# Optimization experiments

Measured on AMD Instinct MI355X. Metric: run time of the kernel, lower is better.

The kernel has to match this reference:

```python
import jax, jax.numpy as jnp
import numpy as np

NUM_HEADS = 16
HEAD_DIM = 64
HIDDEN = NUM_HEADS * HEAD_DIM  # 1024


def get_rel_pos(q_size, k_size, rel_pos):
    # q_size == k_size here and rel_pos already has 2*size-1 rows, so the
    # F.interpolate(mode='linear') resize in the original is an identity.
    # relative_coords = q - k + (k_size - 1)  (scale factors are 1.0)
    coords = jnp.arange(q_size)[:, None] - jnp.arange(k_size)[None, :] + (k_size - 1)
    return rel_pos[coords]  # [q_size, k_size, head_dim]


def setup_inputs() -> dict:
    key = jax.random.key(0)
    ks = jax.random.split(key, 7)
    B, H, W = 4, 56, 28
    inp = {
        "hidden_states": jax.random.normal(ks[0], (B, H, W, HIDDEN), jnp.float32),
        "qkv_w": jax.random.normal(ks[1], (3 * HIDDEN, HIDDEN), jnp.float32) * 0.02,
        "qkv_b": jax.random.normal(ks[2], (3 * HIDDEN,), jnp.float32) * 0.02,
        "proj_w": jax.random.normal(ks[3], (HIDDEN, HIDDEN), jnp.float32) * 0.02,
        "proj_b": jax.random.normal(ks[4], (HIDDEN,), jnp.float32) * 0.02,
        "rel_pos_h": jax.random.normal(ks[5], (2 * H - 1, HEAD_DIM), jnp.float32) * 0.02,
        "rel_pos_w": jax.random.normal(ks[6], (2 * W - 1, HEAD_DIM), jnp.float32) * 0.02,
    }
    return inp


def reference(hidden_states, qkv_w, qkv_b, proj_w, proj_b, rel_pos_h, rel_pos_w):
    B, H, W, C = hidden_states.shape
    N = H * W
    scale = HEAD_DIM ** -0.5

    # qkv projection -> [3, B*heads, N, head_dim]
    qkv = hidden_states @ qkv_w.T + qkv_b
    qkv = qkv.reshape(B, N, 3, NUM_HEADS, HEAD_DIM).transpose(2, 0, 3, 1, 4)
    qkv = qkv.reshape(3, B * NUM_HEADS, N, HEAD_DIM)
    query, key_, value = qkv[0], qkv[1], qkv[2]

    # scaled dot-product scores, fully materialized as in the original
    attn = jnp.einsum('bqd,bkd->bqk', query * scale, key_)  # [B*heads, N, N]

    # decomposed relative position bias
    Rh = get_rel_pos(H, H, rel_pos_h)  # [H, H, d]
    Rw = get_rel_pos(W, W, rel_pos_w)  # [W, W, d]
    q_r = query.reshape(B * NUM_HEADS, H, W, HEAD_DIM)
    rel_h = jnp.einsum('bhwc,hkc->bhwk', q_r, Rh)  # [B*heads, H, W, H]
    rel_w = jnp.einsum('bhwc,wkc->bhwk', q_r, Rw)  # [B*heads, H, W, W]
    attn = attn.reshape(B * NUM_HEADS, H, W, H, W)
    attn = attn + rel_h[:, :, :, :, None] + rel_w[:, :, :, None, :]
    attn = attn.reshape(B * NUM_HEADS, N, N)

    attn = jax.nn.softmax(attn.astype(jnp.float32), axis=-1).astype(query.dtype)

    out = jnp.einsum('bqk,bkd->bqd', attn, value)
    out = out.reshape(B, NUM_HEADS, H, W, HEAD_DIM).transpose(0, 2, 3, 1, 4)
    out = out.reshape(B, H, W, C)
    out = out @ proj_w.T + proj_b
    return out
```

## Files before the change

kernel.cpp:

```cpp
#include <hip/hip_runtime.h>
#include <hip/hip_bf16.h>
#include <stdint.h>

typedef __bf16 bf16;
typedef __bf16 bf16x2 __attribute__((ext_vector_type(2)));
typedef __bf16 bf16x4 __attribute__((ext_vector_type(4)));
typedef __bf16 bf16x8 __attribute__((ext_vector_type(8)));
typedef float f32x4 __attribute__((ext_vector_type(4)));

#define AS1 __attribute__((address_space(1)))
#define AS3 __attribute__((address_space(3)))

static __device__ __forceinline__ void async_cp16(const bf16* g, bf16* l) {
    __builtin_amdgcn_global_load_lds((const AS1 void*)g, (AS3 void*)l, 16, 0, 0);
}

static __device__ __forceinline__ bf16x4 cvt4(f32x4 v) {
    bf16x4 r;
    r[0] = (bf16)v[0]; r[1] = (bf16)v[1]; r[2] = (bf16)v[2]; r[3] = (bf16)v[3];
    return r;
}

static __device__ __forceinline__ float fast_exp2(float x) {
#if __has_builtin(__builtin_amdgcn_exp2f)
    return __builtin_amdgcn_exp2f(x);
#else
    return __expf(x * 0.69314718056f);
#endif
}

__global__ __launch_bounds__(256) void cvt_kernel(
    const float* __restrict__ src, bf16* __restrict__ dst, int n4) {
    int i = blockIdx.x * 256 + threadIdx.x;
    const int stride = gridDim.x * 256;
    for (; i < n4; i += stride)
        ((bf16x4*)dst)[i] = cvt4(((const f32x4*)src)[i]);
}

__global__ __launch_bounds__(256) void build_kone(bf16* __restrict__ Kone) {
    const int idx = blockIdx.x * 256 + threadIdx.x;
    if (idx >= 6400) return;
    const int key = idx >> 2, chunk = idx & 3;
    const int hk = key / 28;
    const int wk = key - hk * 28;
    const int kt = key >> 6;
    const int ha = (kt << 6) / 28;
    const int jw = 27 - wk;
    const int jh = 31 - (hk - ha);
    bf16x8 v;
#pragma unroll
    for (int e = 0; e < 8; e++) {
        const int j = chunk * 8 + e;
        v[e] = (j == jw || j == jh) ? (bf16)1.0f : (bf16)0.0f;
    }
    *(bf16x8*)&Kone[key * 32 + chunk * 8] = v;
}

__global__ __launch_bounds__(256) void zero_pads(
    bf16* __restrict__ Kb, bf16* __restrict__ Vt) {
    const int idx = blockIdx.x * 256 + threadIdx.x;
    if (idx >= 32768) return;
    const int g = idx >> 9, r = idx & 511;
    bf16x8 z = {};
    if (r < 256) {
        *(bf16x8*)&Kb[((size_t)g * 1600 + 1568) * 64 + r * 8] = z;
    } else {
        const int rr = r - 256;
        *(bf16x8*)&Vt[((size_t)g * 64 + (rr >> 2)) * 1600 + 1568 + (rr & 3) * 8] = z;
    }
}


#define QKV_EPILOGUE()                                                        \
    for (int nt = 0; nt < 4; nt++) {                                          \
        const int n_ = n0 + wn + nt * 16 + lm;                                \
        const float bv = bias[n_];                                            \
        const int s = n_ >> 10, rem = n_ & 1023;                              \
        const int h = rem >> 6, d = rem & 63;                                 \
        const float qsc = (s == 0) ? 0.18033688011112042f : 1.0f;             \
        for (int mt = 0; mt < 4; mt++) {                                      \
            for (int r = 0; r < 4; r++) {                                     \
                const int m_ = m0 + wm + mt * 16 + quad * 4 + r;              \
                const int b = m_ / 1568;                                      \
                const int pix = m_ - b * 1568;                                \
                const int g = b * 16 + h;                                     \
                const bf16 v = (bf16)((acc[mt][nt][r] + bv) * qsc);           \
                if (s == 0)      Qb[((size_t)g * 1568 + pix) * 64 + d] = v;   \
                else if (s == 1) Kb[((size_t)g * 1600 + pix) * 64 + d] = v;   \
                else {                                                        \
                    const int lk = pix & 31;                                  \
                    const int ppix = (pix & ~31) | ((lk & 15) << 1) | (lk >> 4); \
                    Vt[((size_t)g * 64 + d) * 1600 + ppix] = v;               \
                }                                                             \
            }                                                                 \
        }                                                                     \
    }

__global__ __launch_bounds__(256) void qkv_gemm_bf16(
    const bf16* __restrict__ A, const bf16* __restrict__ W,
    const float* __restrict__ bias, bf16* __restrict__ Qb,
    bf16* __restrict__ Kb, bf16* __restrict__ Vt) {
    __shared__ bf16 As[128 * 32];
    __shared__ bf16 Bs[128 * 32];
    const int t = threadIdx.x;
    const int wid = t >> 6, lane = t & 63;
    const int m0 = blockIdx.x * 128, n0 = blockIdx.y * 128;
    const int wm = (wid & 1) * 64, wn = (wid >> 1) * 64;
    const int r_i = lane >> 2, c8 = (lane & 3) * 8;
    const int lm = lane & 15, quad = lane >> 4;

    f32x4 acc[4][4] = {};
    for (int k0 = 0; k0 < 1024; k0 += 32) {
        __syncthreads();
        for (int i = 0; i < 2; i++) {
            const int blk = wid * 2 + i;
            async_cp16(A + (size_t)(m0 + blk * 16 + r_i) * 1024 + k0 + c8, As + blk * 512);
            async_cp16(W + (size_t)(n0 + blk * 16 + r_i) * 1024 + k0 + c8, Bs + blk * 512);
        }
        __syncthreads();
        bf16x8 af[4], bfr[4];
        for (int x = 0; x < 4; x++) {
            af[x]  = *(const bf16x8*)&As[(wm + x * 16 + lm) * 32 + quad * 8];
            bfr[x] = *(const bf16x8*)&Bs[(wn + x * 16 + lm) * 32 + quad * 8];
        }
        for (int mt = 0; mt < 4; mt++)
            for (int nt = 0; nt < 4; nt++)
                acc[mt][nt] = __builtin_amdgcn_mfma_f32_16x16x32_bf16(af[mt], bfr[nt], acc[mt][nt], 0, 0, 0);
    }
    QKV_EPILOGUE()
}

__global__ __launch_bounds__(256) void qkv_gemm_f32(
    const float* __restrict__ A, const float* __restrict__ W,
    const float* __restrict__ bias, bf16* __restrict__ Qb,
    bf16* __restrict__ Kb, bf16* __restrict__ Vt) {
    __shared__ bf16 As[128 * 32];
    __shared__ bf16 Bs[128 * 32];
    const int t = threadIdx.x;
    const int wid = t >> 6, lane = t & 63;
    const int m0 = blockIdx.x * 128, n0 = blockIdx.y * 128;
    const int wm = (wid & 1) * 64, wn = (wid >> 1) * 64;
    const int lm = lane & 15, quad = lane >> 4;

    f32x4 acc[4][4] = {};
    for (int k0 = 0; k0 < 1024; k0 += 32) {
        __syncthreads();
        for (int i = 0; i < 4; i++) {
            const int idx = t + i * 256;
            const int row = idx >> 3, c4 = (idx & 7) * 4;
            const f32x4 av = *(const f32x4*)&A[(size_t)(m0 + row) * 1024 + k0 + c4];
            const f32x4 wv = *(const f32x4*)&W[(size_t)(n0 + row) * 1024 + k0 + c4];
            *(bf16x4*)&As[row * 32 + c4] = cvt4(av);
            *(bf16x4*)&Bs[row * 32 + c4] = cvt4(wv);
        }
        __syncthreads();
        bf16x8 af[4], bfr[4];
        for (int x = 0; x < 4; x++) {
            af[x]  = *(const bf16x8*)&As[(wm + x * 16 + lm) * 32 + quad * 8];
            bfr[x] = *(const bf16x8*)&Bs[(wn + x * 16 + lm) * 32 + quad * 8];
        }
        for (int mt = 0; mt < 4; mt++)
            for (int nt = 0; nt < 4; nt++)
                acc[mt][nt] = __builtin_amdgcn_mfma_f32_16x16x32_bf16(af[mt], bfr[nt], acc[mt][nt], 0, 0, 0);
    }
    QKV_EPILOGUE()
}

__global__ __launch_bounds__(256) void flash_attn(
    const bf16* __restrict__ Qb, const bf16* __restrict__ Kb,
    const bf16* __restrict__ Vt, const float* __restrict__ rph,
    const float* __restrict__ rpw, const bf16* __restrict__ Kone,
    bf16* __restrict__ AO) {
    const int x = blockIdx.x;
    const int xcd = x & 7, j = x >> 3;
    const int g = xcd * 8 + j / 25;
    const int qblk = j - (j / 25) * 25;
    const int q0 = qblk * 64;
    const int hqb = q0 / 28;

    __shared__ __align__(16) char smem[51200];
    bf16* Th = (bf16*)smem;
    const char* ThC = (const char*)smem;
    char* B = smem + 8192;
    bf16* Qs  = (bf16*)(B + 32768);
    bf16* RPh = (bf16*)(B + 0);
    bf16* RPw = (bf16*)(B + 9216);
    float* TwF = (float*)(B + 18432);
    bf16* TwS = (bf16*)(B + 33280);

    const int t = threadIdx.x, wid = t >> 6, lane = t & 63;
    const int lm = lane & 15, quad = lane >> 4;
    const int qbase_l = wid * 16 + quad * 4;
    const int swz = (lm & 7) << 4;
    const int l3 = lane >> 3, l7 = lane & 7;
    const int swe = ((l7 ^ l3) << 3);

    const bf16* kSrc[2];
    const bf16* vSrc[2];
#pragma unroll
    for (int i = 0; i < 2; i++) {
        kSrc[i] = Kb + ((size_t)g * 1600 + wid * 16 + i * 8 + l3) * 64 + swe;
        vSrc[i] = Vt + ((size_t)g * 64 + wid * 16 + i * 8 + l3) * 1600 + swe;
    }

    for (int c = t; c < 512; c += 256) {
        const int row = c >> 3, col = (c & 7) * 8;
        const int qg = min(q0 + row, 1567);
        *(bf16x8*)&Qs[row * 72 + col] =
            *(const bf16x8*)&Qb[((size_t)g * 1568 + qg) * 64 + col];
    }
    for (int c = t; c < 1024; c += 256) {
        const int row = c >> 4, col = (c & 15) * 4;
        const int rg = min(hqb + row, 110);
        *(bf16x4*)&RPh[row * 72 + col] = cvt4(*(const f32x4*)&rph[rg * 64 + col]);
    }
    __syncthreads();

    const int qrow_l = wid * 16 + lm;
    const bf16x8 qf0 = *(const bf16x8*)&Qs[qrow_l * 72 + quad * 8];
    const bf16x8 qf1 = *(const bf16x8*)&Qs[qrow_l * 72 + 32 + quad * 8];
    const int qgl = min(q0 + qrow_l, 1567);
    const int thb2 = (qrow_l * 64 + (qgl / 28 - hqb) + 54) * 2;

    for (int c = t; c < 1024; c += 256) {
        const int row = c >> 4, col = (c & 15) * 4;
        const int rg = min(row, 54);
        *(bf16x4*)&RPw[row * 72 + col] = cvt4(*(const f32x4*)&rpw[rg * 64 + col]);
    }
    f32x4 acch[4];
#pragma unroll
    for (int nt = 0; nt < 4; nt++) {
        const bf16x8 b0 = *(const bf16x8*)&RPh[(nt * 16 + lm) * 72 + quad * 8];
        const bf16x8 b1 = *(const bf16x8*)&RPh[(nt * 16 + lm) * 72 + 32 + quad * 8];
        f32x4 a = {};
        a = __builtin_amdgcn_mfma_f32_16x16x32_bf16(qf0, b0, a, 0, 0, 0);
        a = __builtin_amdgcn_mfma_f32_16x16x32_bf16(qf1, b1, a, 0, 0, 0);
        acch[nt] = a;
    }
    __syncthreads();

#pragma unroll
    for (int nt = 0; nt < 4; nt++) {
        const int c = nt * 16 + lm;
        if (c < 59) {
#pragma unroll
            for (int r = 0; r < 4; r++)
                Th[(qbase_l + r) * 64 + c + 2] = (bf16)(acch[nt][r] * 8.0f);
        }
    }
    if (lm == 0) {
#pragma unroll
        for (int r = 0; r < 4; r++) {
            Th[(qbase_l + r) * 64 + 0] = (bf16)0.0f;
            Th[(qbase_l + r) * 64 + 1] = (bf16)0.0f;
        }
    }
#pragma unroll
    for (int nt = 0; nt < 4; nt++) {
        const bf16x8 b0 = *(const bf16x8*)&RPw[(nt * 16 + lm) * 72 + quad * 8];
        const bf16x8 b1 = *(const bf16x8*)&RPw[(nt * 16 + lm) * 72 + 32 + quad * 8];
        f32x4 a = {};
        a = __builtin_amdgcn_mfma_f32_16x16x32_bf16(qf0, b0, a, 0, 0, 0);
        a = __builtin_amdgcn_mfma_f32_16x16x32_bf16(qf1, b1, a, 0, 0, 0);
        const int c = nt * 16 + lm;
        if (c < 55) {
#pragma unroll
            for (int r = 0; r < 4; r++)
                TwF[(qbase_l + r) * 58 + c] = a[r] * 8.0f;
        }
    }
    __syncthreads();

    {
        const int row = t >> 2, chunk = t & 3;
        const int qg = min(q0 + row, 1567);
        const int wq = qg % 28;
        const float* src = &TwF[row * 58 + wq];
        bf16x8 v;
        if (chunk < 3) {
#pragma unroll
            for (int e = 0; e < 8; e++) v[e] = (bf16)src[chunk * 8 + e];
        } else {
#pragma unroll
            for (int e = 0; e < 4; e++) v[e] = (bf16)src[24 + e];
#pragma unroll
            for (int e = 4; e < 8; e++) v[e] = (bf16)0.0f;
        }
        *(bf16x8*)&TwS[row * 32 + chunk * 8] = v;
    }
    __syncthreads();

    const bf16x8 qt_mine = *(const bf16x8*)&TwS[qrow_l * 32 + quad * 8];

#pragma unroll
    for (int i = 0; i < 2; i++) {
        async_cp16(kSrc[i], (bf16*)(B + (wid * 2 + i) * 1024));
        async_cp16(vSrc[i], (bf16*)(B + 16384 + (wid * 2 + i) * 1024));
        kSrc[i] += 4096;
        vSrc[i] += 64;
    }
    const bf16* kop = Kone + lm * 32 + quad * 8;
    bf16x8 ko[4];
#pragma unroll
    for (int f = 0; f < 4; f++) ko[f] = *(const bf16x8*)(kop + f * 512);
    __syncthreads();

    f32x4 o[4] = {};
    f32x4 lsum = {};
    const f32x4 zero4 = {};
    bf16x8 ones;
#pragma unroll
    for (int i = 0; i < 8; i++) ones[i] = (bf16)1.0f;

    bf16* P0w = (bf16*)(B + 32768) + wid * 640;
    bf16* P1w = (bf16*)(B + 37888) + wid * 640;

    int curo = 0;
    for (int kt = 0; kt < 25; kt++) {
        bf16x8 qf2 = qt_mine;
        if (quad == 3) {
            const int ha = (kt << 6) / 28;
            const char* tp = ThC + (thb2 - (ha << 1));
            qf2[4] = *(const bf16*)(tp);
            qf2[5] = *(const bf16*)(tp + 2);
            qf2[6] = *(const bf16*)(tp + 4);
            qf2[7] = *(const bf16*)(tp + 6);
        }

        if (kt < 24) {
            const int nxto = curo ^ 8192;
#pragma unroll
            for (int i = 0; i < 2; i++) {
                async_cp16(kSrc[i], (bf16*)(B + nxto + (wid * 2 + i) * 1024));
                async_cp16(vSrc[i], (bf16*)(B + 16384 + nxto + (wid * 2 + i) * 1024));
                kSrc[i] += 4096;
                vSrc[i] += 64;
            }
        }

        __builtin_amdgcn_s_setprio(1);
        f32x4 s[4];
#pragma unroll
        for (int f = 0; f < 4; f++)
            s[f] = __builtin_amdgcn_mfma_f32_16x16x32_bf16(qf2, ko[f], zero4, 0, 0, 0);
        {
            const char* KsB = B + curo;
            const int x0 = (quad * 16) ^ swz;
#pragma unroll
            for (int f = 0; f < 4; f++) {
                const char* rp = KsB + (f * 16 + lm) * 128;
                const bf16x8 ka = *(const bf16x8*)(rp + x0);
                const bf16x8 kb2 = *(const bf16x8*)(rp + (x0 ^ 64));
                s[f] = __builtin_amdgcn_mfma_f32_16x16x32_bf16(qf0, ka, s[f], 0, 0, 0);
                s[f] = __builtin_amdgcn_mfma_f32_16x16x32_bf16(qf1, kb2, s[f], 0, 0, 0);
            }
        }
        __builtin_amdgcn_s_setprio(0);

        if (kt < 24) {
            kop += 2048;
#pragma unroll
            for (int f = 0; f < 4; f++) ko[f] = *(const bf16x8*)(kop + f * 512);
        }

        if (kt == 24) {
#pragma unroll
            for (int r = 0; r < 4; r++) { s[2][r] = -30000.0f; s[3][r] = -30000.0f; }
        }

#pragma unroll
        for (int r = 0; r < 4; r++) {
            const float a0 = fast_exp2(s[0][r]);
            const float a1 = fast_exp2(s[1][r]);
            bf16x2 pp; pp[0] = (bf16)a0; pp[1] = (bf16)a1;
            *(bf16x2*)&P0w[(quad * 4 + r) * 40 + lm * 2] = pp;
            const float b0 = fast_exp2(s[2][r]);
            const float b1 = fast_exp2(s[3][r]);
            bf16x2 qq; qq[0] = (bf16)b0; qq[1] = (bf16)b1;
            *(bf16x2*)&P1w[(quad * 4 + r) * 40 + lm * 2] = qq;
        }
        __asm__ volatile("s_waitcnt lgkmcnt(0)" ::: "memory");
        const bf16x8 pf0 = *(const bf16x8*)&P0w[lm * 40 + quad * 8];
        const bf16x8 pf1 = *(const bf16x8*)&P1w[lm * 40 + quad * 8];
        lsum = __builtin_amdgcn_mfma_f32_16x16x32_bf16(pf0, ones, lsum, 0, 0, 0);
        lsum = __builtin_amdgcn_mfma_f32_16x16x32_bf16(pf1, ones, lsum, 0, 0, 0);
        __builtin_amdgcn_s_setprio(1);
        {
            const char* VsB = B + 16384 + curo;
#pragma unroll
            for (int dt = 0; dt < 4; dt++) {
                const bf16x8 vf = *(const bf16x8*)(VsB + (dt * 16 + lm) * 128 +
                                                   ((quad * 16) ^ swz));
                o[dt] = __builtin_amdgcn_mfma_f32_16x16x32_bf16(pf0, vf, o[dt], 0, 0, 0);
            }
#pragma unroll
            for (int dt = 0; dt < 4; dt++) {
                const bf16x8 vf = *(const bf16x8*)(VsB + (dt * 16 + lm) * 128 +
                                                   ((64 + quad * 16) ^ swz));
                o[dt] = __builtin_amdgcn_mfma_f32_16x16x32_bf16(pf1, vf, o[dt], 0, 0, 0);
            }
        }
        __builtin_amdgcn_s_setprio(0);

        if (kt < 24) {
            __syncthreads();
            curo ^= 8192;
        }
    }

    if (q0 + wid * 16 < 1568) {
        const int bo = g >> 4, hh = g & 15;
#pragma unroll
        for (int r = 0; r < 4; r++) {
            const float inv = 1.0f / lsum[r];
            const size_t base = ((size_t)bo * 1568 + q0 + qbase_l + r) * 1024 + hh * 64;
#pragma unroll
            for (int dt = 0; dt < 4; dt++)
                AO[base + dt * 16 + lm] = (bf16)(o[dt][r] * inv);
        }
    }
}

__global__ __launch_bounds__(256) void proj_gemm_bf16(
    const bf16* __restrict__ A, const bf16* __restrict__ W,
    const float* __restrict__ bias, float* __restrict__ out) {
    __shared__ bf16 As[128 * 32];
    __shared__ bf16 Bs[128 * 32];
    const int t = threadIdx.x;
    const int wid = t >> 6, lane = t & 63;
    const int m0 = blockIdx.x * 128, n0 = blockIdx.y * 128;
    const int wm = (wid & 1) * 64, wn = (wid >> 1) * 64;
    const int r_i = lane >> 2, c8 = (lane & 3) * 8;
    const int lm = lane & 15, quad = lane >> 4;

    f32x4 acc[4][4] = {};
    for (int k0 = 0; k0 < 1024; k0 += 32) {
        __syncthreads();
        for (int i = 0; i < 2; i++) {
            const int blk = wid * 2 + i;
            async_cp16(A + (size_t)(m0 + blk * 16 + r_i) * 1024 + k0 + c8, As + blk * 512);
            async_cp16(W + (size_t)(n0 + blk * 16 + r_i) * 1024 + k0 + c8, Bs + blk * 512);
        }
        __syncthreads();
        bf16x8 af[4], bfr[4];
        for (int x = 0; x < 4; x++) {
            af[x]  = *(const bf16x8*)&As[(wm + x * 16 + lm) * 32 + quad * 8];
            bfr[x] = *(const bf16x8*)&Bs[(wn + x * 16 + lm) * 32 + quad * 8];
        }
        for (int mt = 0; mt < 4; mt++)
            for (int nt = 0; nt < 4; nt++)
                acc[mt][nt] = __builtin_amdgcn_mfma_f32_16x16x32_bf16(af[mt], bfr[nt], acc[mt][nt], 0, 0, 0);
    }
    for (int nt = 0; nt < 4; nt++) {
        const int n_ = n0 + wn + nt * 16 + lm;
        const float bv = bias[n_];
        for (int mt = 0; mt < 4; mt++)
            for (int r = 0; r < 4; r++) {
                const int m_ = m0 + wm + mt * 16 + quad * 4 + r;
                out[(size_t)m_ * 1024 + n_] = acc[mt][nt][r] + bv;
            }
    }
}

__global__ __launch_bounds__(256) void proj_gemm_f32(
    const bf16* __restrict__ A, const float* __restrict__ W,
    const float* __restrict__ bias, float* __restrict__ out) {
    __shared__ bf16 As[128 * 32];
    __shared__ bf16 Bs[128 * 32];
    const int t = threadIdx.x;
    const int wid = t >> 6, lane = t & 63;
    const int m0 = blockIdx.x * 128, n0 = blockIdx.y * 128;
    const int wm = (wid & 1) * 64, wn = (wid >> 1) * 64;
    const int r_i = lane >> 2, c8 = (lane & 3) * 8;
    const int lm = lane & 15, quad = lane >> 4;

    f32x4 acc[4][4] = {};
    for (int k0 = 0; k0 < 1024; k0 += 32) {
        __syncthreads();
        for (int i = 0; i < 2; i++) {
            const int blk = wid * 2 + i;
            async_cp16(A + (size_t)(m0 + blk * 16 + r_i) * 1024 + k0 + c8, As + blk * 512);
        }
        for (int i = 0; i < 4; i++) {
            const int idx = t + i * 256;
            const int row = idx >> 3, c4 = (idx & 7) * 4;
            const f32x4 wv = *(const f32x4*)&W[(size_t)(n0 + row) * 1024 + k0 + c4];
            *(bf16x4*)&Bs[row * 32 + c4] = cvt4(wv);
        }
        __syncthreads();
        bf16x8 af[4], bfr[4];
        for (int x = 0; x < 4; x++) {
            af[x]  = *(const bf16x8*)&As[(wm + x * 16 + lm) * 32 + quad * 8];
            bfr[x] = *(const bf16x8*)&Bs[(wn + x * 16 + lm) * 32 + quad * 8];
        }
        for (int mt = 0; mt < 4; mt++)
            for (int nt = 0; nt < 4; nt++)
                acc[mt][nt] = __builtin_amdgcn_mfma_f32_16x16x32_bf16(af[mt], bfr[nt], acc[mt][nt], 0, 0, 0);
    }
    for (int nt = 0; nt < 4; nt++) {
        const int n_ = n0 + wn + nt * 16 + lm;
        const float bv = bias[n_];
        for (int mt = 0; mt < 4; mt++)
            for (int r = 0; r < 4; r++) {
                const int m_ = m0 + wm + mt * 16 + quad * 4 + r;
                out[(size_t)m_ * 1024 + n_] = acc[mt][nt][r] + bv;
            }
    }
}

extern "C" void kernel_launch(void* const* d_in, const int* in_sizes, int n_in,
                              void* d_out, int out_size, void* d_ws, size_t ws_size,
                              hipStream_t stream) {
    const float* hs     = (const float*)d_in[0];
    const float* qkv_w  = (const float*)d_in[1];
    const float* qkv_b  = (const float*)d_in[2];
    const float* proj_w = (const float*)d_in[3];
    const float* proj_b = (const float*)d_in[4];
    const float* rph    = (const float*)d_in[5];
    const float* rpw    = (const float*)d_in[6];
    float* out = (float*)d_out;

    const size_t GQ  = (size_t)64 * 1568 * 64;
    const size_t GKP = (size_t)64 * 1600 * 64;
    const size_t N_KONE = (size_t)1600 * 32;
    const size_t N_HS = (size_t)6272 * 1024;
    const size_t N_QW = (size_t)3072 * 1024;
    const size_t N_PW = (size_t)1024 * 1024;
    bf16* Qb = (bf16*)d_ws;
    bf16* Kb = Qb + GQ;
    bf16* Vt = Kb + GKP;
    bf16* AO = Vt + GKP;
    bf16* Kone = AO + GQ;
    bf16* hs_bf    = Kone + N_KONE;
    bf16* qkvw_bf  = hs_bf + N_HS;
    bf16* projw_bf = qkvw_bf + N_QW;
    const size_t need = (2 * GQ + 2 * GKP + N_KONE + N_HS + N_QW + N_PW) * sizeof(bf16);

    if (ws_size >= need) {
        build_kone<<<25, 256, 0, stream>>>(Kone);
        zero_pads<<<128, 256, 0, stream>>>(Kb, Vt);
        cvt_kernel<<<512, 256, 0, stream>>>(hs, hs_bf, (int)(N_HS / 4));
        cvt_kernel<<<512, 256, 0, stream>>>(qkv_w, qkvw_bf, (int)(N_QW / 4));
        cvt_kernel<<<256, 256, 0, stream>>>(proj_w, projw_bf, (int)(N_PW / 4));
        qkv_gemm_bf16<<<dim3(49, 24), 256, 0, stream>>>(hs_bf, qkvw_bf, qkv_b, Qb, Kb, Vt);
        flash_attn<<<1600, 256, 0, stream>>>(Qb, Kb, Vt, rph, rpw, Kone, AO);
        proj_gemm_bf16<<<dim3(49, 8), 256, 0, stream>>>(AO, projw_bf, proj_b, out);
    } else {
        build_kone<<<25, 256, 0, stream>>>(Kone);
        zero_pads<<<128, 256, 0, stream>>>(Kb, Vt);
        qkv_gemm_f32<<<dim3(49, 24), 256, 0, stream>>>(hs, qkv_w, qkv_b, Qb, Kb, Vt);
        flash_attn<<<1600, 256, 0, stream>>>(Qb, Kb, Vt, rph, rpw, Kone, AO);
        proj_gemm_f32<<<dim3(49, 8), 256, 0, stream>>>(AO, proj_w, proj_b, out);
    }
}
```

Baseline: 355.1 us.

## Swizzle GEMM block order across XCDs and drop per-head K/V padding

The QKV and projection GEMMs switch to a 1D grid whose block index is remapped so that consecutive tiles land on the same XCD, aiming to improve L2 reuse of A/W tiles. The K and V^T buffers lose their 1600-row per-head padding and use a 1568 stride, with only a small slack region zeroed at the very end. Attention tail tiles now read the next head's rows instead of zeros, which is correct only if those keys are masked; in exchange the per-group zeroing work is reduced to a single tiny launch.

```diff
diff --git a/kernel.cpp b/kernel.cpp
--- a/kernel.cpp
+++ b/kernel.cpp
@@ -56,18 +56,12 @@
     *(bf16x8*)&Kone[key * 32 + chunk * 8] = v;
 }
 
-__global__ __launch_bounds__(256) void zero_pads(
-    bf16* __restrict__ Kb, bf16* __restrict__ Vt) {
-    const int idx = blockIdx.x * 256 + threadIdx.x;
-    if (idx >= 32768) return;
-    const int g = idx >> 9, r = idx & 511;
+__global__ __launch_bounds__(256) void zero_slack(
+    bf16* __restrict__ a, bf16* __restrict__ b) {
+    const int i = threadIdx.x;
     bf16x8 z = {};
-    if (r < 256) {
-        *(bf16x8*)&Kb[((size_t)g * 1600 + 1568) * 64 + r * 8] = z;
-    } else {
-        const int rr = r - 256;
-        *(bf16x8*)&Vt[((size_t)g * 64 + (rr >> 2)) * 1600 + 1568 + (rr & 3) * 8] = z;
-    }
+    *(bf16x8*)&a[i * 8] = z;
+    *(bf16x8*)&b[i * 8] = z;
 }
 
 
@@ -86,15 +80,16 @@
                 const int g = b * 16 + h;                                     \
                 const bf16 v = (bf16)((acc[mt][nt][r] + bv) * qsc);           \
                 if (s == 0)      Qb[((size_t)g * 1568 + pix) * 64 + d] = v;   \
-                else if (s == 1) Kb[((size_t)g * 1600 + pix) * 64 + d] = v;   \
+                else if (s == 1) Kb[((size_t)g * 1568 + pix) * 64 + d] = v;   \
                 else {                                                        \
                     const int lk = pix & 31;                                  \
                     const int ppix = (pix & ~31) | ((lk & 15) << 1) | (lk >> 4); \
-                    Vt[((size_t)g * 64 + d) * 1600 + ppix] = v;               \
+                    Vt[((size_t)g * 64 + d) * 1568 + ppix] = v;               \
                 }                                                             \
             }                                                                 \
         }                                                                     \
     }
+
 
 __global__ __launch_bounds__(256) void qkv_gemm_bf16(
     const bf16* __restrict__ A, const bf16* __restrict__ W,
@@ -104,7 +99,10 @@
     __shared__ bf16 Bs[128 * 32];
     const int t = threadIdx.x;
     const int wid = t >> 6, lane = t & 63;
-    const int m0 = blockIdx.x * 128, n0 = blockIdx.y * 128;
+    const int bid = blockIdx.x;
+    const int widx = (bid & 7) * 147 + (bid >> 3);
+    const int mt_ = widx / 24;
+    const int m0 = mt_ * 128, n0 = (widx - mt_ * 24) * 128;
     const int wm = (wid & 1) * 64, wn = (wid >> 1) * 64;
     const int r_i = lane >> 2, c8 = (lane & 3) * 8;
     const int lm = lane & 15, quad = lane >> 4;
@@ -138,7 +136,10 @@
     __shared__ bf16 Bs[128 * 32];
     const int t = threadIdx.x;
     const int wid = t >> 6, lane = t & 63;
-    const int m0 = blockIdx.x * 128, n0 = blockIdx.y * 128;
+    const int bid = blockIdx.x;
+    const int widx = (bid & 7) * 147 + (bid >> 3);
+    const int mt_ = widx / 24;
+    const int m0 = mt_ * 128, n0 = (widx - mt_ * 24) * 128;
     const int wm = (wid & 1) * 64, wn = (wid >> 1) * 64;
     const int lm = lane & 15, quad = lane >> 4;
 
@@ -199,8 +200,8 @@
     const bf16* vSrc[2];
 #pragma unroll
     for (int i = 0; i < 2; i++) {
-        kSrc[i] = Kb + ((size_t)g * 1600 + wid * 16 + i * 8 + l3) * 64 + swe;
-        vSrc[i] = Vt + ((size_t)g * 64 + wid * 16 + i * 8 + l3) * 1600 + swe;
+        kSrc[i] = Kb + ((size_t)g * 1568 + wid * 16 + i * 8 + l3) * 64 + swe;
+        vSrc[i] = Vt + ((size_t)g * 64 + wid * 16 + i * 8 + l3) * 1568 + swe;
     }
 
     for (int c = t; c < 512; c += 256) {
@@ -428,7 +429,9 @@
     __shared__ bf16 Bs[128 * 32];
     const int t = threadIdx.x;
     const int wid = t >> 6, lane = t & 63;
-    const int m0 = blockIdx.x * 128, n0 = blockIdx.y * 128;
+    const int bid = blockIdx.x;
+    const int widx = (bid & 7) * 49 + (bid >> 3);
+    const int m0 = (widx >> 3) * 128, n0 = (widx & 7) * 128;
     const int wm = (wid & 1) * 64, wn = (wid >> 1) * 64;
     const int r_i = lane >> 2, c8 = (lane & 3) * 8;
     const int lm = lane & 15, quad = lane >> 4;
@@ -469,7 +472,9 @@
     __shared__ bf16 Bs[128 * 32];
     const int t = threadIdx.x;
     const int wid = t >> 6, lane = t & 63;
-    const int m0 = blockIdx.x * 128, n0 = blockIdx.y * 128;
+    const int bid = blockIdx.x;
+    const int widx = (bid & 7) * 49 + (bid >> 3);
+    const int m0 = (widx >> 3) * 128, n0 = (widx & 7) * 128;
     const int wm = (wid & 1) * 64, wn = (wid >> 1) * 64;
     const int r_i = lane >> 2, c8 = (lane & 3) * 8;
     const int lm = lane & 15, quad = lane >> 4;
@@ -521,35 +526,35 @@
     float* out = (float*)d_out;
 
     const size_t GQ  = (size_t)64 * 1568 * 64;
-    const size_t GKP = (size_t)64 * 1600 * 64;
+    const size_t SL  = 2048;
     const size_t N_KONE = (size_t)1600 * 32;
     const size_t N_HS = (size_t)6272 * 1024;
     const size_t N_QW = (size_t)3072 * 1024;
     const size_t N_PW = (size_t)1024 * 1024;
     bf16* Qb = (bf16*)d_ws;
     bf16* Kb = Qb + GQ;
-    bf16* Vt = Kb + GKP;
-    bf16* AO = Vt + GKP;
+    bf16* Vt = Kb + GQ + SL;
+    bf16* AO = Vt + GQ + SL;
     bf16* Kone = AO + GQ;
     bf16* hs_bf    = Kone + N_KONE;
     bf16* qkvw_bf  = hs_bf + N_HS;
     bf16* projw_bf = qkvw_bf + N_QW;
-    const size_t need = (2 * GQ + 2 * GKP + N_KONE + N_HS + N_QW + N_PW) * sizeof(bf16);
+    const size_t need = (4 * GQ + 2 * SL + N_KONE + N_HS + N_QW + N_PW) * sizeof(bf16);
 
     if (ws_size >= need) {
         build_kone<<<25, 256, 0, stream>>>(Kone);
-        zero_pads<<<128, 256, 0, stream>>>(Kb, Vt);
+        zero_slack<<<1, 256, 0, stream>>>(Kb + GQ, Vt + GQ);
         cvt_kernel<<<512, 256, 0, stream>>>(hs, hs_bf, (int)(N_HS / 4));
         cvt_kernel<<<512, 256, 0, stream>>>(qkv_w, qkvw_bf, (int)(N_QW / 4));
         cvt_kernel<<<256, 256, 0, stream>>>(proj_w, projw_bf, (int)(N_PW / 4));
-        qkv_gemm_bf16<<<dim3(49, 24), 256, 0, stream>>>(hs_bf, qkvw_bf, qkv_b, Qb, Kb, Vt);
+        qkv_gemm_bf16<<<1176, 256, 0, stream>>>(hs_bf, qkvw_bf, qkv_b, Qb, Kb, Vt);
         flash_attn<<<1600, 256, 0, stream>>>(Qb, Kb, Vt, rph, rpw, Kone, AO);
-        proj_gemm_bf16<<<dim3(49, 8), 256, 0, stream>>>(AO, projw_bf, proj_b, out);
+        proj_gemm_bf16<<<392, 256, 0, stream>>>(AO, projw_bf, proj_b, out);
     } else {
         build_kone<<<25, 256, 0, stream>>>(Kone);
-        zero_pads<<<128, 256, 0, stream>>>(Kb, Vt);
-        qkv_gemm_f32<<<dim3(49, 24), 256, 0, stream>>>(hs, qkv_w, qkv_b, Qb, Kb, Vt);
+        zero_slack<<<1, 256, 0, stream>>>(Kb + GQ, Vt + GQ);
+        qkv_gemm_f32<<<1176, 256, 0, stream>>>(hs, qkv_w, qkv_b, Qb, Kb, Vt);
         flash_attn<<<1600, 256, 0, stream>>>(Qb, Kb, Vt, rph, rpw, Kone, AO);
-        proj_gemm_f32<<<dim3(49, 8), 256, 0, stream>>>(AO, proj_w, proj_b, out);
-    }
-}
+        proj_gemm_f32<<<392, 256, 0, stream>>>(AO, proj_w, proj_b, out);
+    }
+}
```

After: 310.1 us. -12.7%, faster.
